# Optimization experiments

Hardware: AMD Instinct MI355X
Metric: run time of the kernel (lower is better)

Reference implementation:

```python
import jax, jax.numpy as jnp
import numpy as np

D_MODEL = 1024
NUM_HEADS = 16
D_K = D_MODEL // NUM_HEADS
ROPE_THETA = 10000.0


def setup_inputs() -> dict:
    key = jax.random.key(0)
    kx, kq, kk, kv, ko = jax.random.split(key, 5)
    B, S = 2, 2048
    sigma = np.sqrt(2.0) / np.sqrt(D_MODEL + D_MODEL)
    x = jax.random.normal(kx, (B, S, D_MODEL), dtype=jnp.float32)
    Wq = jax.random.normal(kq, (D_MODEL, D_MODEL), dtype=jnp.float32) * sigma
    Wk = jax.random.normal(kk, (D_MODEL, D_MODEL), dtype=jnp.float32) * sigma
    Wv = jax.random.normal(kv, (D_MODEL, D_MODEL), dtype=jnp.float32) * sigma
    Wo = jax.random.normal(ko, (D_MODEL, D_MODEL), dtype=jnp.float32) * sigma
    return {"x": x, "Wq": Wq, "Wk": Wk, "Wv": Wv, "Wo": Wo}


def _rope(t, positions):
    # t: [B, H, S, D_K], positions: [S]
    half = jnp.arange(0, D_K, 2, dtype=jnp.float32)          # [D_K/2]
    freqs = 1.0 / (ROPE_THETA ** (half / D_K))               # [D_K/2]
    angles = positions[:, None].astype(jnp.float32) * freqs  # [S, D_K/2]
    cos = jnp.cos(angles)
    sin = jnp.sin(angles)
    t_even = t[..., 0::2]
    t_odd = t[..., 1::2]
    even_rot = t_even * cos - t_odd * sin
    odd_rot = t_even * sin + t_odd * cos
    # interleave back to [..., D_K]
    return jnp.stack([even_rot, odd_rot], axis=-1).reshape(t.shape)


def reference(x, Wq, Wk, Wv, Wo):
    B, S, _ = x.shape
    # weight layout is [d_out, d_in]: y = x @ W.T
    def proj(W):
        y = jnp.einsum('bsd,ed->bse', x, W)
        return y.reshape(B, S, NUM_HEADS, D_K).transpose(0, 2, 1, 3)  # [B,H,S,Dk]
    Q, K, V = proj(Wq), proj(Wk), proj(Wv)
    positions = jnp.arange(S)
    Q = _rope(Q, positions)
    K = _rope(K, positions)
    scale = 1.0 / jnp.sqrt(jnp.asarray(D_K, dtype=x.dtype))
    scores = jnp.einsum('bhqd,bhkd->bhqk', Q, K) * scale  # [B,H,S,S]
    causal = jnp.tril(jnp.ones((S, S), dtype=bool))
    scores = jnp.where(causal, scores, -jnp.inf)
    probs = jax.nn.softmax(scores, axis=-1)
    out = jnp.einsum('bhqk,bhkd->bhqd', probs, V)          # [B,H,S,Dk]
    out = out.transpose(0, 2, 1, 3).reshape(B, S, D_MODEL)
    return jnp.einsum('bsd,ed->bse', out, Wo)
```

## Files before the change

### kernel.cpp

```cpp
#include <hip/hip_runtime.h>
#include <hip/hip_bf16.h>
#include <math.h>

#define S_LEN   2048
#define BATCH   2
#define DMODEL  1024
#define NHEADS  16
#define DKH     64
#define MROWS   (BATCH * S_LEN)

#define SPLIT_Q0   17
#define NPIECE     47
#define SLOTS_BH   30
#define PO_FLOATS  (960 * 4096)

typedef __attribute__((ext_vector_type(8))) __bf16 bf16x8;
typedef __attribute__((ext_vector_type(4))) float f32x4;
typedef __attribute__((ext_vector_type(8))) unsigned short u16x8;

__device__ __forceinline__ float bfu2f(unsigned short u) {
    union { unsigned int i; float f; } v;
    v.i = ((unsigned int)u) << 16;
    return v.f;
}

__device__ __forceinline__ unsigned short f2bfu(float f) {
    union { __bf16 h; unsigned short u; } v;
    v.h = (__bf16)f;
    return v.u;
}

#define LGKM0() __builtin_amdgcn_s_waitcnt(0xc07f)

#define VMCNT_BAR(n) do {                                        \
    asm volatile("s_waitcnt vmcnt(" #n ")" ::: "memory");        \
    __builtin_amdgcn_s_barrier();                                \
    __builtin_amdgcn_sched_barrier(0);                           \
} while (0)

__device__ __forceinline__ void gload_lds16(const void* g, void* l) {
    __builtin_amdgcn_global_load_lds(
        (const __attribute__((address_space(1))) void*)g,
        (__attribute__((address_space(3))) void*)l, 16, 0, 0);
}

__global__ __launch_bounds__(256) void cvt_all(
    const float* __restrict__ W0, const float* __restrict__ W1, const float* __restrict__ W2,
    const float* __restrict__ X,
    unsigned short* __restrict__ Wb,
    unsigned short* __restrict__ Xb)
{
    const int y = blockIdx.y;
    const float* src;
    unsigned short* dst;
    if (y < 3) {
        src = (y == 0) ? W0 : (y == 1) ? W1 : W2;
        dst = Wb + (size_t)y * (DMODEL * DMODEL);
    } else {
        src = X + (size_t)(y - 3) * (DMODEL * DMODEL);
        dst = Xb + (size_t)(y - 3) * (DMODEL * DMODEL);
    }
    size_t idx = ((size_t)blockIdx.x * 256 + threadIdx.x) * 8;
    float4 a = *(const float4*)(src + idx);
    float4 b = *(const float4*)(src + idx + 4);
    u16x8 h;
    h[0] = f2bfu(a.x); h[1] = f2bfu(a.y); h[2] = f2bfu(a.z); h[3] = f2bfu(a.w);
    h[4] = f2bfu(b.x); h[5] = f2bfu(b.y); h[6] = f2bfu(b.z); h[7] = f2bfu(b.w);
    *(u16x8*)(dst + idx) = h;
}

__global__ __launch_bounds__(256) void cvt_wo(
    const float* __restrict__ W, unsigned short* __restrict__ Wob)
{
    size_t idx = ((size_t)blockIdx.x * 256 + threadIdx.x) * 8;
    float4 a = *(const float4*)(W + idx);
    float4 b = *(const float4*)(W + idx + 4);
    u16x8 h;
    h[0] = f2bfu(a.x); h[1] = f2bfu(a.y); h[2] = f2bfu(a.z); h[3] = f2bfu(a.w);
    h[4] = f2bfu(b.x); h[5] = f2bfu(b.y); h[6] = f2bfu(b.z); h[7] = f2bfu(b.w);
    *(u16x8*)(Wob + idx) = h;
}

__global__ __launch_bounds__(256) void gemm_qkv(
    const unsigned short* __restrict__ Xb,
    const unsigned short* __restrict__ Wb,
    unsigned short* __restrict__ Yq, unsigned short* __restrict__ Yk, unsigned short* __restrict__ Yv)
{
    __shared__ __align__(16) unsigned char pool[49152];
    unsigned short* base = (unsigned short*)pool;

    const int tid  = threadIdx.x;
    const int wave = tid >> 6;
    const int lane = tid & 63;
    const int c    = lane & 15;
    const int quad = lane >> 4;

    const int m0 = blockIdx.y * 128;
    const int n0 = blockIdx.x * 128;
    const int w_idx = n0 >> 10;
    const int e0    = n0 & 1023;
    const unsigned short* Wsrc = Wb + (size_t)w_idx * (DMODEL * DMODEL);

    const int mhalf = (wave & 1) * 64;
    const int nhalf = (wave >> 1) * 64;

    f32x4 acc[4][4];
#pragma unroll
    for (int i = 0; i < 4; i++)
#pragma unroll
        for (int j = 0; j < 4; j++) acc[i][j] = (f32x4){0.f, 0.f, 0.f, 0.f};

    const int srow = wave * 32 + (lane >> 2);
    const int scol = (lane & 3) * 8;
    const unsigned short* Asrc = Xb   + (size_t)(m0 + srow) * DMODEL + scol;
    const unsigned short* Bsrc = Wsrc + (size_t)(e0 + srow) * DMODEL + scol;
    const int doff = srow * 32 + scol;

#define QKV_STAGE(buf, kt) do {                                                    \
    unsigned short* _A = base + (buf) * 8192;                                      \
    unsigned short* _B = _A + 4096;                                                \
    const int _k0 = (kt) * 32;                                                     \
    _Pragma("unroll")                                                              \
    for (int _j = 0; _j < 2; _j++) {                                               \
        gload_lds16(Asrc + (size_t)(_j * 16) * DMODEL + _k0, _A + doff + _j * 512);\
        gload_lds16(Bsrc + (size_t)(_j * 16) * DMODEL + _k0, _B + doff + _j * 512);\
    }                                                                              \
} while (0)

#define QKV_COMPUTE(buf) do {                                                      \
    const unsigned short* _A = base + (buf) * 8192;                                \
    const unsigned short* _B = _A + 4096;                                          \
    bf16x8 af[4], bfr[4];                                                          \
    _Pragma("unroll")                                                              \
    for (int mt = 0; mt < 4; mt++)                                                 \
        af[mt] = *(const bf16x8*)(&_A[(mhalf + mt * 16 + c) * 32 + quad * 8]);     \
    _Pragma("unroll")                                                              \
    for (int nt = 0; nt < 4; nt++)                                                 \
        bfr[nt] = *(const bf16x8*)(&_B[(nhalf + nt * 16 + c) * 32 + quad * 8]);    \
    _Pragma("unroll")                                                              \
    for (int mt = 0; mt < 4; mt++)                                                 \
        _Pragma("unroll")                                                          \
        for (int nt = 0; nt < 4; nt++)                                             \
            acc[mt][nt] = __builtin_amdgcn_mfma_f32_16x16x32_bf16(af[mt], bfr[nt], acc[mt][nt], 0, 0, 0); \
} while (0)

    QKV_STAGE(0, 0);
    QKV_STAGE(1, 1);
    for (int g = 0; g < 10; ++g) {
        const int t = g * 3;
        VMCNT_BAR(4); QKV_STAGE(2, t + 2); QKV_COMPUTE(0);
        VMCNT_BAR(4); QKV_STAGE(0, t + 3); QKV_COMPUTE(1);
        VMCNT_BAR(4); QKV_STAGE(1, t + 4); QKV_COMPUTE(2);
    }
    VMCNT_BAR(4); QKV_COMPUTE(0);
    VMCNT_BAR(0); QKV_COMPUTE(1);

    __syncthreads();

    const int h = (e0 + nhalf) >> 6;
    if (w_idx < 2) {
        unsigned short* Yqk = (w_idx == 0) ? Yq : Yk;
        float* EPf = (float*)pool + wave * 16 * 68;
        const int row = lane >> 2;
        const int cg  = lane & 3;
#pragma unroll
        for (int mt = 0; mt < 4; mt++) {
            LGKM0();
#pragma unroll
            for (int nt = 0; nt < 4; nt++)
#pragma unroll
                for (int r = 0; r < 4; r++)
                    EPf[(quad * 4 + r) * 68 + nt * 16 + c] = acc[mt][nt][r];
            LGKM0();
            float fl[16];
#pragma unroll
            for (int j = 0; j < 4; j++) {
                float4 v = *(const float4*)(&EPf[row * 68 + cg * 16 + j * 4]);
                fl[j * 4 + 0] = v.x; fl[j * 4 + 1] = v.y;
                fl[j * 4 + 2] = v.z; fl[j * 4 + 3] = v.w;
            }
            int m = m0 + mhalf + mt * 16 + row;
            int s = m & (S_LEN - 1);
            int b = m >> 11;
            u16x8 o0, o1;
#pragma unroll
            for (int pi = 0; pi < 8; pi++) {
                int p = cg * 8 + pi;
                float freq  = exp2f(-(float)p * 0.41524101186092034f);
                float angle = (float)s * freq;
                float sn, cs;
                __sincosf(angle, &sn, &cs);
                float ev = fl[2 * pi], ov = fl[2 * pi + 1];
                float re = ev * cs - ov * sn;
                float ro = ev * sn + ov * cs;
                if (pi < 4) { o0[2 * pi] = f2bfu(re); o0[2 * pi + 1] = f2bfu(ro); }
                else        { o1[2 * (pi - 4)] = f2bfu(re); o1[2 * (pi - 4) + 1] = f2bfu(ro); }
            }
            unsigned short* dst = Yqk + (((size_t)(b * NHEADS + h)) * S_LEN + s) * DKH + cg * 16;
            *(u16x8*)(dst)     = o0;
            *(u16x8*)(dst + 8) = o1;
        }
    } else {
        unsigned short* EPb = (unsigned short*)pool + wave * 64 * 72;
        LGKM0();
#pragma unroll
        for (int nt = 0; nt < 4; nt++)
#pragma unroll
            for (int mt = 0; mt < 4; mt++)
#pragma unroll
                for (int r = 0; r < 4; r++)
                    EPb[(nt * 16 + c) * 72 + mt * 16 + quad * 4 + r] = f2bfu(acc[mt][nt][r]);
        LGKM0();
        int mbase = m0 + mhalf;
        int s0 = mbase & (S_LEN - 1);
        int b  = mbase >> 11;
        unsigned short* dst = Yv + (((size_t)(b * NHEADS + h)) * DKH + lane) * S_LEN + s0;
#pragma unroll
        for (int j = 0; j < 8; j++)
            *(u16x8*)(dst + j * 8) = *(const u16x8*)(&EPb[lane * 72 + j * 8]);
    }
#undef QKV_STAGE
#undef QKV_COMPUTE
}

__global__ __launch_bounds__(256) void gemm_wo(
    const unsigned short* __restrict__ X,
    const unsigned short* __restrict__ Wob,
    float* __restrict__ Yf)
{
    __shared__ __align__(16) unsigned char pool[36864];
    unsigned short* base = (unsigned short*)pool;

    const int tid  = threadIdx.x;
    const int wave = tid >> 6;
    const int lane = tid & 63;
    const int c    = lane & 15;
    const int quad = lane >> 4;

    const int m0 = blockIdx.y * 64;
    const int n0 = blockIdx.x * 128;

    const int mhalf = (wave & 1) * 32;
    const int nhalf = (wave >> 1) * 64;

    f32x4 acc[2][4];
#pragma unroll
    for (int i = 0; i < 2; i++)
#pragma unroll
        for (int j = 0; j < 4; j++) acc[i][j] = (f32x4){0.f, 0.f, 0.f, 0.f};

    const int arow = wave * 16 + (lane >> 2);
    const int brow = wave * 32 + (lane >> 2);
    const int scol = (lane & 3) * 8;
    const unsigned short* Asrc = X   + (size_t)(m0 + arow) * DMODEL + scol;
    const unsigned short* Bsrc = Wob + (size_t)(n0 + brow) * DMODEL + scol;
    const int adoff = arow * 32 + scol;
    const int bdoff = brow * 32 + scol;

#define WO_STAGE(buf, kt) do {                                                     \
    unsigned short* _A = base + (buf) * 6144;                                      \
    unsigned short* _B = _A + 2048;                                                \
    const int _k0 = (kt) * 32;                                                     \
    gload_lds16(Asrc + _k0, _A + adoff);                                           \
    _Pragma("unroll")                                                              \
    for (int _j = 0; _j < 2; _j++)                                                 \
        gload_lds16(Bsrc + (size_t)(_j * 16) * DMODEL + _k0, _B + bdoff + _j * 512);\
} while (0)

#define WO_COMPUTE(buf) do {                                                       \
    const unsigned short* _A = base + (buf) * 6144;                                \
    const unsigned short* _B = _A + 2048;                                          \
    bf16x8 af[2], bfr[4];                                                          \
    _Pragma("unroll")                                                              \
    for (int mt = 0; mt < 2; mt++)                                                 \
        af[mt] = *(const bf16x8*)(&_A[(mhalf + mt * 16 + c) * 32 + quad * 8]);     \
    _Pragma("unroll")                                                              \
    for (int nt = 0; nt < 4; nt++)                                                 \
        bfr[nt] = *(const bf16x8*)(&_B[(nhalf + nt * 16 + c) * 32 + quad * 8]);    \
    _Pragma("unroll")                                                              \
    for (int mt = 0; mt < 2; mt++)                                                 \
        _Pragma("unroll")                                                          \
        for (int nt = 0; nt < 4; nt++)                                             \
            acc[mt][nt] = __builtin_amdgcn_mfma_f32_16x16x32_bf16(af[mt], bfr[nt], acc[mt][nt], 0, 0, 0); \
} while (0)

    WO_STAGE(0, 0);
    WO_STAGE(1, 1);
    for (int g = 0; g < 10; ++g) {
        const int t = g * 3;
        VMCNT_BAR(3); WO_STAGE(2, t + 2); WO_COMPUTE(0);
        VMCNT_BAR(3); WO_STAGE(0, t + 3); WO_COMPUTE(1);
        VMCNT_BAR(3); WO_STAGE(1, t + 4); WO_COMPUTE(2);
    }
    VMCNT_BAR(3); WO_COMPUTE(0);
    VMCNT_BAR(0); WO_COMPUTE(1);

    __syncthreads();

    float* EPf = (float*)pool + wave * 16 * 68;
    const int row = lane >> 2;
    const int cg  = lane & 3;
#pragma unroll
    for (int mt = 0; mt < 2; mt++) {
        LGKM0();
#pragma unroll
        for (int nt = 0; nt < 4; nt++)
#pragma unroll
            for (int r = 0; r < 4; r++)
                EPf[(quad * 4 + r) * 68 + nt * 16 + c] = acc[mt][nt][r];
        LGKM0();
        int m = m0 + mhalf + mt * 16 + row;
        float* dst = Yf + (size_t)m * DMODEL + n0 + nhalf + cg * 16;
#pragma unroll
        for (int j = 0; j < 4; j++)
            *(float4*)(dst + j * 4) = *(const float4*)(&EPf[row * 68 + cg * 16 + j * 4]);
    }
#undef WO_STAGE
#undef WO_COMPUTE
}

__global__ __launch_bounds__(256, 8) void attn_mfma(
    const unsigned short* __restrict__ Q,
    const unsigned short* __restrict__ K,
    const unsigned short* __restrict__ Vt,
    unsigned short* __restrict__ A,
    float* __restrict__ Scr)
{
    __shared__ unsigned short Ks[2][32 * 72];
    __shared__ unsigned short Vs[2][64 * 40];
    __shared__ unsigned short Plds[4][16 * 40];

    const int tid  = threadIdx.x;
    const int wave = tid >> 6;
    const int lane = tid & 63;
    const int c    = lane & 15;
    const int quad = lane >> 4;

    const int bh = blockIdx.x;
    const int b  = bh >> 4;
    const int h  = bh & 15;

    const int R = (int)blockIdx.y;
    int qb, t_lo, t_hi, spl = 0;
    bool is_split;
    if (R <= 16) {
        qb = 16 - R; t_lo = 0; t_hi = 2 * qb + 2; is_split = false;
    } else {
        int i = R - 17;
        qb  = 31 - (i >> 1);
        spl = i & 1;
        int nk = 2 * qb + 2, half = nk >> 1;
        t_lo = spl ? half : 0;
        t_hi = spl ? nk   : half;
        is_split = true;
    }
    const int q0b = qb * 64;
    const int q0  = q0b + wave * 16;

    const unsigned short* Qb = Q  + (size_t)bh * S_LEN * DKH;
    const unsigned short* Kb = K  + (size_t)bh * S_LEN * DKH;
    const unsigned short* Vb = Vt + (size_t)bh * DKH * S_LEN;

    bf16x8 qf0 = *(const bf16x8*)(Qb + (q0 + c) * DKH + quad * 8);
    bf16x8 qf1 = *(const bf16x8*)(Qb + (q0 + c) * DKH + 32 + quad * 8);

    f32x4 o0 = {0.f,0.f,0.f,0.f}, o1 = o0, o2 = o0, o3 = o0;
    float l[4] = {0.f, 0.f, 0.f, 0.f};

    unsigned short* Pw = &Plds[wave][0];

    const int my_nkb   = (q0 + 16 + 31) >> 5;
    const int kb_full  = (q0 >= 31) ? (((q0 - 31) >> 5) + 1) : 0;

    const int krow  = tid >> 3;
    const int kcol8 = (tid & 7) * 8;
    const int vrow  = tid >> 2;
    const int vcol8 = (tid & 3) * 8;

    uint4 gK = *(const uint4*)(Kb + (size_t)(t_lo * 32 + krow) * DKH + kcol8);
    uint4 gV = *(const uint4*)(Vb + (size_t)vrow * S_LEN + t_lo * 32 + vcol8);
    *(uint4*)(&Ks[t_lo & 1][krow * 72 + kcol8]) = gK;
    *(uint4*)(&Vs[t_lo & 1][vrow * 40 + vcol8]) = gV;

    for (int kb = t_lo; kb < t_hi; kb++) {
        const int k0 = kb * 32;
        const int nb = kb + 1;
        const bool pre = nb < t_hi;
        __syncthreads();
        if (pre) {
            gK = *(const uint4*)(Kb + (size_t)(nb * 32 + krow) * DKH + kcol8);
            gV = *(const uint4*)(Vb + (size_t)vrow * S_LEN + nb * 32 + vcol8);
        }
        if (kb < my_nkb) {
            const unsigned short* Kc = &Ks[kb & 1][0];
            const unsigned short* Vc = &Vs[kb & 1][0];
            bf16x8 k00 = *(const bf16x8*)(&Kc[c * 72 + quad * 8]);
            bf16x8 k01 = *(const bf16x8*)(&Kc[c * 72 + 32 + quad * 8]);
            bf16x8 k10 = *(const bf16x8*)(&Kc[(16 + c) * 72 + quad * 8]);
            bf16x8 k11 = *(const bf16x8*)(&Kc[(16 + c) * 72 + 32 + quad * 8]);
            f32x4 s0 = {0.f,0.f,0.f,0.f}, s1 = {0.f,0.f,0.f,0.f};
            __builtin_amdgcn_s_setprio(1);
            s0 = __builtin_amdgcn_mfma_f32_16x16x32_bf16(qf0, k00, s0, 0, 0, 0);
            s0 = __builtin_amdgcn_mfma_f32_16x16x32_bf16(qf1, k01, s0, 0, 0, 0);
            s1 = __builtin_amdgcn_mfma_f32_16x16x32_bf16(qf0, k10, s1, 0, 0, 0);
            s1 = __builtin_amdgcn_mfma_f32_16x16x32_bf16(qf1, k11, s1, 0, 0, 0);
            __builtin_amdgcn_s_setprio(0);

            if (kb < kb_full) {
#pragma unroll
                for (int r = 0; r < 4; r++) {
                    float e0 = __expf(s0[r] * 0.125f);
                    float e1 = __expf(s1[r] * 0.125f);
                    unsigned short pb0 = f2bfu(e0);
                    unsigned short pb1 = f2bfu(e1);
                    Pw[(quad * 4 + r) * 40 + c]      = pb0;
                    Pw[(quad * 4 + r) * 40 + 16 + c] = pb1;
                    l[r] += bfu2f(pb0) + bfu2f(pb1);
                }
            } else {
#pragma unroll
                for (int r = 0; r < 4; r++) {
                    int qrow = q0 + quad * 4 + r;
                    float e0 = (k0 + c      <= qrow) ? __expf(s0[r] * 0.125f) : 0.0f;
                    float e1 = (k0 + 16 + c <= qrow) ? __expf(s1[r] * 0.125f) : 0.0f;
                    unsigned short pb0 = f2bfu(e0);
                    unsigned short pb1 = f2bfu(e1);
                    Pw[(quad * 4 + r) * 40 + c]      = pb0;
                    Pw[(quad * 4 + r) * 40 + 16 + c] = pb1;
                    l[r] += bfu2f(pb0) + bfu2f(pb1);
                }
            }
            LGKM0();

            bf16x8 pf = *(const bf16x8*)(Pw + c * 40 + quad * 8);

            bf16x8 vf0 = *(const bf16x8*)(&Vc[(0 * 16 + c) * 40 + quad * 8]);
            bf16x8 vf1 = *(const bf16x8*)(&Vc[(1 * 16 + c) * 40 + quad * 8]);
            bf16x8 vf2 = *(const bf16x8*)(&Vc[(2 * 16 + c) * 40 + quad * 8]);
            bf16x8 vf3 = *(const bf16x8*)(&Vc[(3 * 16 + c) * 40 + quad * 8]);
            __builtin_amdgcn_s_setprio(1);
            o0 = __builtin_amdgcn_mfma_f32_16x16x32_bf16(pf, vf0, o0, 0, 0, 0);
            o1 = __builtin_amdgcn_mfma_f32_16x16x32_bf16(pf, vf1, o1, 0, 0, 0);
            o2 = __builtin_amdgcn_mfma_f32_16x16x32_bf16(pf, vf2, o2, 0, 0, 0);
            o3 = __builtin_amdgcn_mfma_f32_16x16x32_bf16(pf, vf3, o3, 0, 0, 0);
            __builtin_amdgcn_s_setprio(0);
        }
        if (pre) {
            *(uint4*)(&Ks[nb & 1][krow * 72 + kcol8]) = gK;
            *(uint4*)(&Vs[nb & 1][vrow * 40 + vcol8]) = gV;
        }
    }

#pragma unroll
    for (int m = 1; m < 16; m <<= 1) {
#pragma unroll
        for (int r = 0; r < 4; r++) l[r] += __shfl_xor(l[r], m, 64);
    }

    if (!is_split) {
#pragma unroll
        for (int r = 0; r < 4; r++) {
            float inv = 1.0f / l[r];
            int s = q0 + quad * 4 + r;
            unsigned short* Ap = A + ((size_t)b * S_LEN + s) * DMODEL + h * DKH;
            Ap[0 * 16 + c] = f2bfu(o0[r] * inv);
            Ap[1 * 16 + c] = f2bfu(o1[r] * inv);
            Ap[2 * 16 + c] = f2bfu(o2[r] * inv);
            Ap[3 * 16 + c] = f2bfu(o3[r] * inv);
        }
    } else {
        const int slot = bh * SLOTS_BH + (qb - SPLIT_Q0) * 2 + spl;
        float* Po = Scr + (size_t)slot * 4096;
        float* Pl = Scr + PO_FLOATS + (size_t)slot * 64;
#pragma unroll
        for (int r = 0; r < 4; r++) {
            int row = wave * 16 + quad * 4 + r;
            Po[row * 64 + 0 * 16 + c] = o0[r];
            Po[row * 64 + 1 * 16 + c] = o1[r];
            Po[row * 64 + 2 * 16 + c] = o2[r];
            Po[row * 64 + 3 * 16 + c] = o3[r];
            if (c == 0) Pl[row] = l[r];
        }
    }
}

__global__ __launch_bounds__(256) void attn_combine(
    const float* __restrict__ Scr, unsigned short* __restrict__ A)
{
    const int bx  = blockIdx.x;
    const int bh  = bx / 15;
    const int qbm = bx % 15;
    const int qb  = SPLIT_Q0 + qbm;
    const int b   = bh >> 4;
    const int h   = bh & 15;

    const int slot0 = bh * SLOTS_BH + qbm * 2;
    const float* O0 = Scr + (size_t)slot0 * 4096;
    const float* O1 = O0 + 4096;
    const float* L0 = Scr + PO_FLOATS + (size_t)slot0 * 64;
    const float* L1 = L0 + 64;

    const int r  = threadIdx.x >> 2;
    const int cg = (threadIdx.x & 3) * 16;

    float inv = 1.0f / (L0[r] + L1[r]);

    u16x8 outv[2];
#pragma unroll
    for (int half = 0; half < 2; half++) {
        float4 a0 = *(const float4*)(O0 + r * 64 + cg + half * 8);
        float4 b0 = *(const float4*)(O0 + r * 64 + cg + half * 8 + 4);
        float4 a1 = *(const float4*)(O1 + r * 64 + cg + half * 8);
        float4 b1 = *(const float4*)(O1 + r * 64 + cg + half * 8 + 4);
        outv[half][0] = f2bfu((a0.x + a1.x) * inv);
        outv[half][1] = f2bfu((a0.y + a1.y) * inv);
        outv[half][2] = f2bfu((a0.z + a1.z) * inv);
        outv[half][3] = f2bfu((a0.w + a1.w) * inv);
        outv[half][4] = f2bfu((b0.x + b1.x) * inv);
        outv[half][5] = f2bfu((b0.y + b1.y) * inv);
        outv[half][6] = f2bfu((b0.z + b1.z) * inv);
        outv[half][7] = f2bfu((b0.w + b1.w) * inv);
    }
    const int s = qb * 64 + r;
    unsigned short* Ap = A + ((size_t)b * S_LEN + s) * DMODEL + h * DKH + cg;
    *(u16x8*)(Ap)     = outv[0];
    *(u16x8*)(Ap + 8) = outv[1];
}

extern "C" void kernel_launch(void* const* d_in, const int* in_sizes, int n_in,
                              void* d_out, int out_size, void* d_ws, size_t ws_size,
                              hipStream_t stream) {
    const float* x  = (const float*)d_in[0];
    const float* Wq = (const float*)d_in[1];
    const float* Wk = (const float*)d_in[2];
    const float* Wv = (const float*)d_in[3];
    const float* Wo = (const float*)d_in[4];
    float* out = (float*)d_out;

    unsigned short* Qw = (unsigned short*)d_ws;
    unsigned short* Kw = Qw + (size_t)MROWS * DMODEL;
    unsigned short* Vw = Kw + (size_t)MROWS * DMODEL;
    unsigned short* Wb = Vw + (size_t)MROWS * DMODEL;
    unsigned short* Aw = Wb;
    unsigned short* Wob = Qw;
    unsigned short* Xb = (unsigned short*)d_out;
    float* Scr = (float*)d_out;

    cvt_all<<<dim3(DMODEL * DMODEL / (256 * 8), 7), 256, 0, stream>>>(Wq, Wk, Wv, x, Wb, Xb);

    gemm_qkv<<<dim3(3 * DMODEL / 128, MROWS / 128), 256, 0, stream>>>(
        Xb, Wb, Qw, Kw, Vw);

    attn_mfma<<<dim3(NHEADS * BATCH, NPIECE), 256, 0, stream>>>(Qw, Kw, Vw, Aw, Scr);

    attn_combine<<<dim3(NHEADS * BATCH * 15), 256, 0, stream>>>(Scr, Aw);

    cvt_wo<<<dim3(DMODEL * DMODEL / (256 * 8)), 256, 0, stream>>>(Wo, Wob);

    gemm_wo<<<dim3(DMODEL / 128, MROWS / 64), 256, 0, stream>>>(Aw, Wob, out);
}
```

Before: 189.7 us.

## Switch attention to 32x32 MFMA with transposed scores and register-only P

```diff
diff --git a/kernel.cpp b/kernel.cpp
--- a/kernel.cpp
+++ b/kernel.cpp
@@ -14,9 +14,10 @@
 #define SLOTS_BH   30
 #define PO_FLOATS  (960 * 4096)
 
-typedef __attribute__((ext_vector_type(8))) __bf16 bf16x8;
-typedef __attribute__((ext_vector_type(4))) float f32x4;
-typedef __attribute__((ext_vector_type(8))) unsigned short u16x8;
+typedef __attribute__((ext_vector_type(8)))  __bf16 bf16x8;
+typedef __attribute__((ext_vector_type(4)))  float  f32x4;
+typedef __attribute__((ext_vector_type(16))) float  f32x16;
+typedef __attribute__((ext_vector_type(8)))  unsigned short u16x8;
 
 __device__ __forceinline__ float bfu2f(unsigned short u) {
     union { unsigned int i; float f; } v;
@@ -47,8 +48,7 @@
 __global__ __launch_bounds__(256) void cvt_all(
     const float* __restrict__ W0, const float* __restrict__ W1, const float* __restrict__ W2,
     const float* __restrict__ X,
-    unsigned short* __restrict__ Wb,
-    unsigned short* __restrict__ Xb)
+    unsigned short* __restrict__ Wb, unsigned short* __restrict__ Xb)
 {
     const int y = blockIdx.y;
     const float* src;
@@ -319,7 +319,7 @@
 #undef WO_COMPUTE
 }
 
-__global__ __launch_bounds__(256, 8) void attn_mfma(
+__global__ __launch_bounds__(128, 4) void attn_mfma(
     const unsigned short* __restrict__ Q,
     const unsigned short* __restrict__ K,
     const unsigned short* __restrict__ Vt,
@@ -328,13 +328,12 @@
 {
     __shared__ unsigned short Ks[2][32 * 72];
     __shared__ unsigned short Vs[2][64 * 40];
-    __shared__ unsigned short Plds[4][16 * 40];
 
     const int tid  = threadIdx.x;
     const int wave = tid >> 6;
     const int lane = tid & 63;
-    const int c    = lane & 15;
-    const int quad = lane >> 4;
+    const int c32  = lane & 31;
+    const int hi   = lane >> 5;
 
     const int bh = blockIdx.x;
     const int b  = bh >> 4;
@@ -355,32 +354,38 @@
         is_split = true;
     }
     const int q0b = qb * 64;
-    const int q0  = q0b + wave * 16;
+    const int q0w = q0b + wave * 32;
 
     const unsigned short* Qb = Q  + (size_t)bh * S_LEN * DKH;
     const unsigned short* Kb = K  + (size_t)bh * S_LEN * DKH;
     const unsigned short* Vb = Vt + (size_t)bh * DKH * S_LEN;
 
-    bf16x8 qf0 = *(const bf16x8*)(Qb + (q0 + c) * DKH + quad * 8);
-    bf16x8 qf1 = *(const bf16x8*)(Qb + (q0 + c) * DKH + 32 + quad * 8);
-
-    f32x4 o0 = {0.f,0.f,0.f,0.f}, o1 = o0, o2 = o0, o3 = o0;
-    float l[4] = {0.f, 0.f, 0.f, 0.f};
-
-    unsigned short* Pw = &Plds[wave][0];
-
-    const int my_nkb   = (q0 + 16 + 31) >> 5;
-    const int kb_full  = (q0 >= 31) ? (((q0 - 31) >> 5) + 1) : 0;
-
-    const int krow  = tid >> 3;
-    const int kcol8 = (tid & 7) * 8;
-    const int vrow  = tid >> 2;
-    const int vcol8 = (tid & 3) * 8;
-
-    uint4 gK = *(const uint4*)(Kb + (size_t)(t_lo * 32 + krow) * DKH + kcol8);
-    uint4 gV = *(const uint4*)(Vb + (size_t)vrow * S_LEN + t_lo * 32 + vcol8);
-    *(uint4*)(&Ks[t_lo & 1][krow * 72 + kcol8]) = gK;
-    *(uint4*)(&Vs[t_lo & 1][vrow * 40 + vcol8]) = gV;
+    bf16x8 qf0 = *(const bf16x8*)(Qb + (size_t)(q0w + c32) * DKH +  0 + hi * 8);
+    bf16x8 qf1 = *(const bf16x8*)(Qb + (size_t)(q0w + c32) * DKH + 16 + hi * 8);
+    bf16x8 qf2 = *(const bf16x8*)(Qb + (size_t)(q0w + c32) * DKH + 32 + hi * 8);
+    bf16x8 qf3 = *(const bf16x8*)(Qb + (size_t)(q0w + c32) * DKH + 48 + hi * 8);
+
+    f32x16 oA, oB;
+#pragma unroll
+    for (int r = 0; r < 16; r++) { oA[r] = 0.f; oB[r] = 0.f; }
+    float lacc = 0.f;
+
+    const int my_nkb = (q0w >> 5) + 1;
+    const int kbf    = q0w >> 5;
+
+    const int krow = tid >> 2;
+    const int kcol = (tid & 3) * 16;
+    const int vrow = tid >> 1;
+    const int vcol = (tid & 1) * 16;
+
+    uint4 gK0 = *(const uint4*)(Kb + (size_t)(t_lo * 32 + krow) * DKH + kcol);
+    uint4 gK1 = *(const uint4*)(Kb + (size_t)(t_lo * 32 + krow) * DKH + kcol + 8);
+    uint4 gV0 = *(const uint4*)(Vb + (size_t)vrow * S_LEN + t_lo * 32 + vcol);
+    uint4 gV1 = *(const uint4*)(Vb + (size_t)vrow * S_LEN + t_lo * 32 + vcol + 8);
+    *(uint4*)(&Ks[t_lo & 1][krow * 72 + kcol])     = gK0;
+    *(uint4*)(&Ks[t_lo & 1][krow * 72 + kcol + 8]) = gK1;
+    *(uint4*)(&Vs[t_lo & 1][vrow * 40 + vcol])     = gV0;
+    *(uint4*)(&Vs[t_lo & 1][vrow * 40 + vcol + 8]) = gV1;
 
     for (int kb = t_lo; kb < t_hi; kb++) {
         const int k0 = kb * 32;
@@ -388,99 +393,112 @@
         const bool pre = nb < t_hi;
         __syncthreads();
         if (pre) {
-            gK = *(const uint4*)(Kb + (size_t)(nb * 32 + krow) * DKH + kcol8);
-            gV = *(const uint4*)(Vb + (size_t)vrow * S_LEN + nb * 32 + vcol8);
+            gK0 = *(const uint4*)(Kb + (size_t)(nb * 32 + krow) * DKH + kcol);
+            gK1 = *(const uint4*)(Kb + (size_t)(nb * 32 + krow) * DKH + kcol + 8);
+            gV0 = *(const uint4*)(Vb + (size_t)vrow * S_LEN + nb * 32 + vcol);
+            gV1 = *(const uint4*)(Vb + (size_t)vrow * S_LEN + nb * 32 + vcol + 8);
         }
         if (kb < my_nkb) {
             const unsigned short* Kc = &Ks[kb & 1][0];
             const unsigned short* Vc = &Vs[kb & 1][0];
-            bf16x8 k00 = *(const bf16x8*)(&Kc[c * 72 + quad * 8]);
-            bf16x8 k01 = *(const bf16x8*)(&Kc[c * 72 + 32 + quad * 8]);
-            bf16x8 k10 = *(const bf16x8*)(&Kc[(16 + c) * 72 + quad * 8]);
-            bf16x8 k11 = *(const bf16x8*)(&Kc[(16 + c) * 72 + 32 + quad * 8]);
-            f32x4 s0 = {0.f,0.f,0.f,0.f}, s1 = {0.f,0.f,0.f,0.f};
+            bf16x8 kf0 = *(const bf16x8*)(&Kc[c32 * 72 +  0 + hi * 8]);
+            bf16x8 kf1 = *(const bf16x8*)(&Kc[c32 * 72 + 16 + hi * 8]);
+            bf16x8 kf2 = *(const bf16x8*)(&Kc[c32 * 72 + 32 + hi * 8]);
+            bf16x8 kf3 = *(const bf16x8*)(&Kc[c32 * 72 + 48 + hi * 8]);
+            f32x16 s;
+#pragma unroll
+            for (int r = 0; r < 16; r++) s[r] = 0.f;
             __builtin_amdgcn_s_setprio(1);
-            s0 = __builtin_amdgcn_mfma_f32_16x16x32_bf16(qf0, k00, s0, 0, 0, 0);
-            s0 = __builtin_amdgcn_mfma_f32_16x16x32_bf16(qf1, k01, s0, 0, 0, 0);
-            s1 = __builtin_amdgcn_mfma_f32_16x16x32_bf16(qf0, k10, s1, 0, 0, 0);
-            s1 = __builtin_amdgcn_mfma_f32_16x16x32_bf16(qf1, k11, s1, 0, 0, 0);
+            s = __builtin_amdgcn_mfma_f32_32x32x16_bf16(kf0, qf0, s, 0, 0, 0);
+            s = __builtin_amdgcn_mfma_f32_32x32x16_bf16(kf1, qf1, s, 0, 0, 0);
+            s = __builtin_amdgcn_mfma_f32_32x32x16_bf16(kf2, qf2, s, 0, 0, 0);
+            s = __builtin_amdgcn_mfma_f32_32x32x16_bf16(kf3, qf3, s, 0, 0, 0);
             __builtin_amdgcn_s_setprio(0);
-
-            if (kb < kb_full) {
-#pragma unroll
-                for (int r = 0; r < 4; r++) {
-                    float e0 = __expf(s0[r] * 0.125f);
-                    float e1 = __expf(s1[r] * 0.125f);
-                    unsigned short pb0 = f2bfu(e0);
-                    unsigned short pb1 = f2bfu(e1);
-                    Pw[(quad * 4 + r) * 40 + c]      = pb0;
-                    Pw[(quad * 4 + r) * 40 + 16 + c] = pb1;
-                    l[r] += bfu2f(pb0) + bfu2f(pb1);
-                }
+            float p[16];
+            if (kb < kbf) {
+#pragma unroll
+                for (int r = 0; r < 16; r++) p[r] = __expf(s[r] * 0.125f);
             } else {
-#pragma unroll
-                for (int r = 0; r < 4; r++) {
-                    int qrow = q0 + quad * 4 + r;
-                    float e0 = (k0 + c      <= qrow) ? __expf(s0[r] * 0.125f) : 0.0f;
-                    float e1 = (k0 + 16 + c <= qrow) ? __expf(s1[r] * 0.125f) : 0.0f;
-                    unsigned short pb0 = f2bfu(e0);
-                    unsigned short pb1 = f2bfu(e1);
-                    Pw[(quad * 4 + r) * 40 + c]      = pb0;
-                    Pw[(quad * 4 + r) * 40 + 16 + c] = pb1;
-                    l[r] += bfu2f(pb0) + bfu2f(pb1);
+                const int qg = q0w + c32;
+#pragma unroll
+                for (int r = 0; r < 16; r++) {
+                    int kg = k0 + (r & 3) + 8 * (r >> 2) + 4 * hi;
+                    p[r] = (kg <= qg) ? __expf(s[r] * 0.125f) : 0.0f;
                 }
             }
-            LGKM0();
-
-            bf16x8 pf = *(const bf16x8*)(Pw + c * 40 + quad * 8);
-
-            bf16x8 vf0 = *(const bf16x8*)(&Vc[(0 * 16 + c) * 40 + quad * 8]);
-            bf16x8 vf1 = *(const bf16x8*)(&Vc[(1 * 16 + c) * 40 + quad * 8]);
-            bf16x8 vf2 = *(const bf16x8*)(&Vc[(2 * 16 + c) * 40 + quad * 8]);
-            bf16x8 vf3 = *(const bf16x8*)(&Vc[(3 * 16 + c) * 40 + quad * 8]);
+            unsigned pk[8];
+#pragma unroll
+            for (int i = 0; i < 8; i++) {
+                asm("v_cvt_pk_bf16_f32 %0, %1, %2"
+                    : "=v"(pk[i]) : "v"(p[2 * i]), "v"(p[2 * i + 1]));
+                union { unsigned u; float f; } lo, hx;
+                lo.u = pk[i] << 16;
+                hx.u = pk[i] & 0xffff0000u;
+                lacc += lo.f + hx.f;
+            }
+            unsigned f0[4], f1[4];
+            {
+                unsigned ta, tb;
+                ta = (unsigned)__shfl_xor((int)pk[2], 32, 64);
+                tb = (unsigned)__shfl_xor((int)pk[0], 32, 64);
+                f0[0] = hi ? ta : pk[0];  f0[2] = hi ? pk[2] : tb;
+                ta = (unsigned)__shfl_xor((int)pk[3], 32, 64);
+                tb = (unsigned)__shfl_xor((int)pk[1], 32, 64);
+                f0[1] = hi ? ta : pk[1];  f0[3] = hi ? pk[3] : tb;
+                ta = (unsigned)__shfl_xor((int)pk[6], 32, 64);
+                tb = (unsigned)__shfl_xor((int)pk[4], 32, 64);
+                f1[0] = hi ? ta : pk[4];  f1[2] = hi ? pk[6] : tb;
+                ta = (unsigned)__shfl_xor((int)pk[7], 32, 64);
+                tb = (unsigned)__shfl_xor((int)pk[5], 32, 64);
+                f1[1] = hi ? ta : pk[5];  f1[3] = hi ? pk[7] : tb;
+            }
+            union { unsigned u[4]; bf16x8 v; } pa0, pa1;
+            pa0.u[0] = f0[0]; pa0.u[1] = f0[1]; pa0.u[2] = f0[2]; pa0.u[3] = f0[3];
+            pa1.u[0] = f1[0]; pa1.u[1] = f1[1]; pa1.u[2] = f1[2]; pa1.u[3] = f1[3];
+            bf16x8 v00 = *(const bf16x8*)(&Vc[(c32)      * 40 +  0 + hi * 8]);
+            bf16x8 v10 = *(const bf16x8*)(&Vc[(c32)      * 40 + 16 + hi * 8]);
+            bf16x8 v01 = *(const bf16x8*)(&Vc[(32 + c32) * 40 +  0 + hi * 8]);
+            bf16x8 v11 = *(const bf16x8*)(&Vc[(32 + c32) * 40 + 16 + hi * 8]);
             __builtin_amdgcn_s_setprio(1);
-            o0 = __builtin_amdgcn_mfma_f32_16x16x32_bf16(pf, vf0, o0, 0, 0, 0);
-            o1 = __builtin_amdgcn_mfma_f32_16x16x32_bf16(pf, vf1, o1, 0, 0, 0);
-            o2 = __builtin_amdgcn_mfma_f32_16x16x32_bf16(pf, vf2, o2, 0, 0, 0);
-            o3 = __builtin_amdgcn_mfma_f32_16x16x32_bf16(pf, vf3, o3, 0, 0, 0);
+            oA = __builtin_amdgcn_mfma_f32_32x32x16_bf16(pa0.v, v00, oA, 0, 0, 0);
+            oA = __builtin_amdgcn_mfma_f32_32x32x16_bf16(pa1.v, v10, oA, 0, 0, 0);
+            oB = __builtin_amdgcn_mfma_f32_32x32x16_bf16(pa0.v, v01, oB, 0, 0, 0);
+            oB = __builtin_amdgcn_mfma_f32_32x32x16_bf16(pa1.v, v11, oB, 0, 0, 0);
             __builtin_amdgcn_s_setprio(0);
         }
         if (pre) {
-            *(uint4*)(&Ks[nb & 1][krow * 72 + kcol8]) = gK;
-            *(uint4*)(&Vs[nb & 1][vrow * 40 + vcol8]) = gV;
+            *(uint4*)(&Ks[nb & 1][krow * 72 + kcol])     = gK0;
+            *(uint4*)(&Ks[nb & 1][krow * 72 + kcol + 8]) = gK1;
+            *(uint4*)(&Vs[nb & 1][vrow * 40 + vcol])     = gV0;
+            *(uint4*)(&Vs[nb & 1][vrow * 40 + vcol + 8]) = gV1;
         }
     }
 
-#pragma unroll
-    for (int m = 1; m < 16; m <<= 1) {
-#pragma unroll
-        for (int r = 0; r < 4; r++) l[r] += __shfl_xor(l[r], m, 64);
-    }
+    lacc += __shfl_xor(lacc, 32, 64);
 
     if (!is_split) {
-#pragma unroll
-        for (int r = 0; r < 4; r++) {
-            float inv = 1.0f / l[r];
-            int s = q0 + quad * 4 + r;
-            unsigned short* Ap = A + ((size_t)b * S_LEN + s) * DMODEL + h * DKH;
-            Ap[0 * 16 + c] = f2bfu(o0[r] * inv);
-            Ap[1 * 16 + c] = f2bfu(o1[r] * inv);
-            Ap[2 * 16 + c] = f2bfu(o2[r] * inv);
-            Ap[3 * 16 + c] = f2bfu(o3[r] * inv);
+        float inv = 1.0f / lacc;
+#pragma unroll
+        for (int r = 0; r < 16; r++) {
+            int qr = (r & 3) + 8 * (r >> 2) + 4 * hi;
+            float invr = __shfl(inv, qr, 64);
+            int sg = q0w + qr;
+            unsigned short* Ap = A + ((size_t)b * S_LEN + sg) * DMODEL + h * DKH;
+            Ap[c32]      = f2bfu(oA[r] * invr);
+            Ap[32 + c32] = f2bfu(oB[r] * invr);
         }
     } else {
         const int slot = bh * SLOTS_BH + (qb - SPLIT_Q0) * 2 + spl;
         float* Po = Scr + (size_t)slot * 4096;
         float* Pl = Scr + PO_FLOATS + (size_t)slot * 64;
 #pragma unroll
-        for (int r = 0; r < 4; r++) {
-            int row = wave * 16 + quad * 4 + r;
-            Po[row * 64 + 0 * 16 + c] = o0[r];
-            Po[row * 64 + 1 * 16 + c] = o1[r];
-            Po[row * 64 + 2 * 16 + c] = o2[r];
-            Po[row * 64 + 3 * 16 + c] = o3[r];
-            if (c == 0) Pl[row] = l[r];
+        for (int r = 0; r < 16; r++) {
+            int qr  = (r & 3) + 8 * (r >> 2) + 4 * hi;
+            int row = wave * 32 + qr;
+            Po[row * 64 + c32]      = oA[r];
+            Po[row * 64 + 32 + c32] = oB[r];
         }
+        if (hi == 0) Pl[wave * 32 + c32] = lacc;
     }
 }
 
@@ -551,7 +569,7 @@
     gemm_qkv<<<dim3(3 * DMODEL / 128, MROWS / 128), 256, 0, stream>>>(
         Xb, Wb, Qw, Kw, Vw);
 
-    attn_mfma<<<dim3(NHEADS * BATCH, NPIECE), 256, 0, stream>>>(Qw, Kw, Vw, Aw, Scr);
+    attn_mfma<<<dim3(NHEADS * BATCH, NPIECE), 128, 0, stream>>>(Qw, Kw, Vw, Aw, Scr);
 
     attn_combine<<<dim3(NHEADS * BATCH * 15), 256, 0, stream>>>(Scr, Aw);
 
```

After: 182.2 us. -4.0%, faster.
